# Kernel optimization log

Hardware: AMD Instinct MI355X
Metric: run time of the kernel (lower is better)

The kernel has to match this reference:

```python
import jax, jax.numpy as jnp
import numpy as np

# Model hyperparameters (from init_kwargs)
CHANNEL_COUNT = 32   # C: features per element
MIXTURE_COUNT = 4    # K: number of class distributions
MIXTURE_SIZE = 4     # S: gaussian components per class
EM_ITERS = 3         # fixed EM refinement iterations
LOG2PI = 1.8378770664093453
COV_REG = 1e-4       # covariance diagonal regularizer
EPS = 1e-6


def setup_inputs() -> dict:
    key = jax.random.key(0)
    kf, kl = jax.random.split(key)
    features = jax.random.normal(kf, (4, CHANNEL_COUNT, 65536), dtype=jnp.float32)
    initial_labels = jax.random.randint(kl, (4, 65536), 0, MIXTURE_COUNT, dtype=jnp.int32)
    return {"features": features, "initial_labels": initial_labels}


def reference(features, initial_labels):
    # features: [B, C, N] float; initial_labels: [B, N] int in [0, K)
    B, C, N = features.shape
    K, S = MIXTURE_COUNT, MIXTURE_SIZE
    dt = features.dtype

    # class membership mask [B, K, N]
    mask = jax.nn.one_hot(initial_labels, K, dtype=dt).transpose(0, 2, 1)
    # deterministic initial within-class component assignment: element n -> component n % S
    comp_onehot = jax.nn.one_hot(jnp.arange(N) % S, S, dtype=dt).T  # [S, N]
    r = mask[:, :, None, :] * comp_onehot[None, None]               # [B, K, S, N]

    eye = COV_REG * jnp.eye(C, dtype=dt)
    logp = None
    for _ in range(EM_ITERS):
        # ---- M-step: per-component weight, mean, covariance (sufficient stats) ----
        w = r.sum(-1)                                                # [B, K, S]
        mu = jnp.einsum('bksn,bcn->bksc', r, features) / (w[..., None] + EPS)
        sxx = jnp.einsum('bksn,bcn,bdn->bkscd', r, features, features) / (w[..., None, None] + EPS)
        cov = sxx - jnp.einsum('bksc,bksd->bkscd', mu, mu) + eye     # [B, K, S, C, C]
        prec = jnp.linalg.inv(cov)
        _, logdet = jnp.linalg.slogdet(cov)                          # [B, K, S]
        pi = (w + EPS) / (w.sum(-1, keepdims=True) + S * EPS)        # mixing weights

        # ---- E-step: full-covariance gaussian log-density per element ----
        t = jnp.einsum('bkscd,bdn->bkscn', prec, features)           # [B, K, S, C, N]
        quad = (jnp.einsum('bcn,bkscn->bksn', features, t)
                - 2.0 * jnp.einsum('bksc,bkscn->bksn', mu, t)
                + jnp.einsum('bksc,bkscd,bksd->bks', mu, prec, mu)[..., None])
        logp = jnp.log(pi)[..., None] - 0.5 * (C * LOG2PI + logdet[..., None] + quad)  # [B,K,S,N]
        # responsibilities within each class, restricted to that class's labeled elements
        r = jax.nn.softmax(logp, axis=2) * mask[:, :, None, :]

    # per-class mixture log-likelihood for EVERY element, then posterior over classes
    class_ll = jax.nn.logsumexp(logp, axis=2)        # [B, K, N]
    output_logits = jax.nn.softmax(class_ll, axis=1)  # class assignment probabilities
    return output_logits
```

## Files before the change

### kernel.cpp

```cpp
#include <hip/hip_runtime.h>
#include <hip/hip_fp16.h>
#include <math.h>

#define BB 4
#define CC 32
#define KK 4
#define SS 4
#define NN 65536

constexpr int NCOMP = 64;
constexpr int SSTRIDE = 1088;
constexpr int PSTRIDE = 1128;
constexpr int NB = 128;
constexpr float EPS_ = 1e-6f;
constexpr float COVREG_ = 1e-4f;
constexpr float LOG2PI_C = 1.8378770664093453f;

__device__ constexpr int XOFF_[32] = {
    0,   4,   8,   12,  16,  24,  32,  40,  48,  60,  72,
    84,  96,  112, 128, 144, 160, 180, 200, 220, 240, 264,
    288, 312, 336, 364, 392, 420, 448, 480, 512, 544};

typedef _Float16 half8 __attribute__((ext_vector_type(8)));
typedef _Float16 half4 __attribute__((ext_vector_type(4)));
typedef float floatx4 __attribute__((ext_vector_type(4)));

template <bool ITER0, int CHUNKS>
__global__ __launch_bounds__(256, 2) void gmm_accum_mfma(
    const float* __restrict__ feat, const int* __restrict__ labels,
    const float* __restrict__ resp, float* __restrict__ partials) {
  __shared__ __align__(16) _Float16 fC[32 * 48];
  __shared__ __align__(16) _Float16 respH[4][32];
  __shared__ __align__(16) _Float16 maskH[4][32];

  const int t = threadIdx.x;
  const int b = blockIdx.y;
  const int blk0 = blockIdx.x * (CHUNKS * 32);
  const int k = t >> 6;
  const int l = t & 63;
  const int row16 = l & 15;
  const int kg = l >> 4;

  floatx4 acc[4][7];
#pragma unroll
  for (int s = 0; s < 4; ++s)
#pragma unroll
    for (int j = 0; j < 7; ++j) acc[s][j] = (floatx4){0.f, 0.f, 0.f, 0.f};

  const int cstage = t >> 3;
  const int n4 = (t & 7) * 4;

  float4 pf;
  float4 presp = make_float4(0, 0, 0, 0);
  int plab = 0;
  pf = *(const float4*)(feat + ((size_t)b * CC + cstage) * NN + blk0 + n4);
  if (t < 32) {
    plab = labels[b * NN + blk0 + t];
    if (!ITER0) presp = *(const float4*)(resp + ((size_t)b * NN + blk0 + t) * 4);
  }

  const half8 hz = {0, 0, 0, 0, 0, 0, 0, 0};

  for (int chunk = 0; chunk < CHUNKS; ++chunk) {
    {
      half4 hv;
      hv[0] = (_Float16)pf.x;
      hv[1] = (_Float16)pf.y;
      hv[2] = (_Float16)pf.z;
      hv[3] = (_Float16)pf.w;
      *(half4*)&fC[cstage * 48 + n4] = hv;
    }
    if (t < 32) {
      if (ITER0) {
        const int cmp = (blk0 + chunk * 32 + t) & 3;
        respH[0][t] = (cmp == 0) ? (_Float16)1 : (_Float16)0;
        respH[1][t] = (cmp == 1) ? (_Float16)1 : (_Float16)0;
        respH[2][t] = (cmp == 2) ? (_Float16)1 : (_Float16)0;
        respH[3][t] = (cmp == 3) ? (_Float16)1 : (_Float16)0;
      } else {
        respH[0][t] = (_Float16)presp.x;
        respH[1][t] = (_Float16)presp.y;
        respH[2][t] = (_Float16)presp.z;
        respH[3][t] = (_Float16)presp.w;
      }
      maskH[0][t] = (plab == 0) ? (_Float16)1 : (_Float16)0;
      maskH[1][t] = (plab == 1) ? (_Float16)1 : (_Float16)0;
      maskH[2][t] = (plab == 2) ? (_Float16)1 : (_Float16)0;
      maskH[3][t] = (plab == 3) ? (_Float16)1 : (_Float16)0;
    }
    __syncthreads();

    if (chunk < CHUNKS - 1) {
      const int n0n = blk0 + (chunk + 1) * 32;
      pf = *(const float4*)(feat + ((size_t)b * CC + cstage) * NN + n0n + n4);
      if (t < 32) {
        plab = labels[b * NN + n0n + t];
        if (!ITER0)
          presp = *(const float4*)(resp + ((size_t)b * NN + n0n + t) * 4);
      }
    }

    const half8 ff0 = *(const half8*)&fC[row16 * 48 + kg * 8];
    const half8 ff1 = *(const half8*)&fC[(row16 + 16) * 48 + kg * 8];

    const half8 mh = *(const half8*)&maskH[k][kg * 8];
    const half8 H0 = ff0 * mh;
    const half8 H1 = ff1 * mh;
    const half8 agB = (row16 == 0) ? mh : hz;

#pragma unroll
    for (int s = 0; s < 4; ++s) {
      const half8 rh = *(const half8*)&respH[s][kg * 8];
      const half8 G0 = ff0 * rh;
      const half8 G1 = ff1 * rh;
      const half8 agA = (row16 == 0) ? rh : hz;
      acc[s][0] =
          __builtin_amdgcn_mfma_f32_16x16x32_f16(G0, H0, acc[s][0], 0, 0, 0);
      acc[s][1] =
          __builtin_amdgcn_mfma_f32_16x16x32_f16(G0, H1, acc[s][1], 0, 0, 0);
      acc[s][2] =
          __builtin_amdgcn_mfma_f32_16x16x32_f16(G1, H0, acc[s][2], 0, 0, 0);
      acc[s][3] =
          __builtin_amdgcn_mfma_f32_16x16x32_f16(G1, H1, acc[s][3], 0, 0, 0);
      acc[s][4] =
          __builtin_amdgcn_mfma_f32_16x16x32_f16(G0, agB, acc[s][4], 0, 0, 0);
      acc[s][5] =
          __builtin_amdgcn_mfma_f32_16x16x32_f16(G1, agB, acc[s][5], 0, 0, 0);
      acc[s][6] =
          __builtin_amdgcn_mfma_f32_16x16x32_f16(agA, agB, acc[s][6], 0, 0, 0);
    }
    __syncthreads();
  }

#pragma unroll
  for (int s = 0; s < 4; ++s) {
    float* sg = partials + ((size_t)(b * gridDim.x + blockIdx.x) * 16 +
                            (k * 4 + s)) *
                               SSTRIDE;
    const int dr = kg * 4;
#pragma unroll
    for (int r = 0; r < 4; ++r) {
      sg[(dr + r) * 32 + row16] = acc[s][0][r];
      sg[(dr + r) * 32 + 16 + row16] = acc[s][1][r];
      sg[(16 + dr + r) * 32 + row16] = acc[s][2][r];
      sg[(16 + dr + r) * 32 + 16 + row16] = acc[s][3][r];
    }
    if (row16 == 0) {
#pragma unroll
      for (int r = 0; r < 4; ++r) {
        sg[1024 + dr + r] = acc[s][4][r];
        sg[1024 + 16 + dr + r] = acc[s][5][r];
      }
    }
    if (l == 0) sg[1056] = acc[s][6][0];
  }
}

template <int TILES>
__global__ __launch_bounds__(256, 2) void gmm_fused(
    const float* __restrict__ feat, const int* __restrict__ labels,
    const float* __restrict__ params, float* __restrict__ partials) {
  __shared__ __align__(16) _Float16 fTd[2 * 64 * 56];
  __shared__ __align__(16) _Float16 fCd[2 * 32 * 72];
  __shared__ int4 xlds4[2048];
  __shared__ float zlds[16 * 32];
  __shared__ float c0lds[16];
  __shared__ int lab_lds[2][64];
  __shared__ __align__(16) _Float16 respHd[2][4][64];
  __shared__ __align__(16) _Float16 maskHd[2][4][64];

  const int t = threadIdx.x;
  const int b = blockIdx.y;
  const int blk0 = blockIdx.x * (TILES * 64);
  const int w = t >> 6;
  const int l = t & 63;
  const int row16 = l & 15;
  const int kg = l >> 4;

  for (int idx = t; idx < 2048; idx += 256) {
    const int c = idx >> 7, chunk = idx & 127;
    xlds4[idx] = *(const int4*)((const char*)(params +
                                              (size_t)(b * 16 + c) * PSTRIDE +
                                              612) +
                                chunk * 16);
  }
  for (int idx = t; idx < 16 * 32; idx += 256) {
    zlds[idx] =
        -params[(size_t)(b * 16 + (idx >> 5)) * PSTRIDE + 576 + (idx & 31)];
  }
  if (t < 16) c0lds[t] = params[(size_t)(b * 16 + t) * PSTRIDE + 608];

  const _Float16* xl = (const _Float16*)xlds4;
  const int cload = t >> 4;
  const int i4 = (t & 15) * 4;
  const half8 hz = {0, 0, 0, 0, 0, 0, 0, 0};

  floatx4 acc[4][7];
#pragma unroll
  for (int s = 0; s < 4; ++s)
#pragma unroll
    for (int j = 0; j < 7; ++j) acc[s][j] = (floatx4){0.f, 0.f, 0.f, 0.f};

  float4 pv0 = *(const float4*)(feat + ((size_t)b * CC + cload) * NN + blk0 + i4);
  float4 pv1 =
      *(const float4*)(feat + ((size_t)b * CC + cload + 16) * NN + blk0 + i4);
  int plab = (t < 64) ? labels[b * NN + blk0 + t] : 0;

  for (int tile = 0; tile < TILES; ++tile) {
    const int base = blk0 + tile * 64;
    const int bs = tile & 1;
    _Float16* fT = &fTd[bs * (64 * 56)];
    _Float16* fC = &fCd[bs * (32 * 72)];

    {
      const _Float16 h0x = (_Float16)pv0.x, h0y = (_Float16)pv0.y;
      const _Float16 h0z = (_Float16)pv0.z, h0w = (_Float16)pv0.w;
      const _Float16 h1x = (_Float16)pv1.x, h1y = (_Float16)pv1.y;
      const _Float16 h1z = (_Float16)pv1.z, h1w = (_Float16)pv1.w;
      fT[(i4 + 0) * 56 + cload] = h0x;
      fT[(i4 + 1) * 56 + cload] = h0y;
      fT[(i4 + 2) * 56 + cload] = h0z;
      fT[(i4 + 3) * 56 + cload] = h0w;
      fT[(i4 + 0) * 56 + cload + 16] = h1x;
      fT[(i4 + 1) * 56 + cload + 16] = h1y;
      fT[(i4 + 2) * 56 + cload + 16] = h1z;
      fT[(i4 + 3) * 56 + cload + 16] = h1w;
      half4 a, c2;
      a[0] = h0x; a[1] = h0y; a[2] = h0z; a[3] = h0w;
      c2[0] = h1x; c2[1] = h1y; c2[2] = h1z; c2[3] = h1w;
      *(half4*)&fC[cload * 72 + i4] = a;
      *(half4*)&fC[(cload + 16) * 72 + i4] = c2;
      if (t < 64) lab_lds[bs][t] = plab;
    }
    __syncthreads();

    if (tile < TILES - 1) {
      const int nb2 = base + 64;
      pv0 = *(const float4*)(feat + ((size_t)b * CC + cload) * NN + nb2 + i4);
      pv1 = *(const float4*)(feat + ((size_t)b * CC + cload + 16) * NN + nb2 +
                             i4);
      if (t < 64) plab = labels[b * NN + nb2 + t];
    }

    const half8 bfr = *(const half8*)&fT[(w * 16 + row16) * 56 + kg * 8];
    const int lab = lab_lds[bs][w * 16 + row16];

    float lp0 = 0.f, lp1 = 0.f, lp2 = 0.f, lp3 = 0.f;
#pragma unroll
    for (int c = 0; c < 16; ++c) {
      const half8 a0 = *(const half8*)&xl[c * 1024 + (0 * 64 + l) * 8];
      const half8 a1 = *(const half8*)&xl[c * 1024 + (1 * 64 + l) * 8];
      const floatx4 cin0 = *(const floatx4*)&zlds[c * 32 + kg * 4];
      const floatx4 cin1 = *(const floatx4*)&zlds[c * 32 + 16 + kg * 4];
      floatx4 y0 =
          __builtin_amdgcn_mfma_f32_16x16x32_f16(a0, bfr, cin0, 0, 0, 0);
      floatx4 y1 =
          __builtin_amdgcn_mfma_f32_16x16x32_f16(a1, bfr, cin1, 0, 0, 0);
      float q = 0.f;
      q = fmaf(y0[0], y0[0], q);
      q = fmaf(y0[1], y0[1], q);
      q = fmaf(y0[2], y0[2], q);
      q = fmaf(y0[3], y0[3], q);
      q = fmaf(y1[0], y1[0], q);
      q = fmaf(y1[1], y1[1], q);
      q = fmaf(y1[2], y1[2], q);
      q = fmaf(y1[3], y1[3], q);
      q += __shfl_xor(q, 16);
      q += __shfl_xor(q, 32);
      const float lp = c0lds[c] - 0.5f * q;
      const bool own = (c >> 2) == lab;
      const int s = c & 3;
      lp0 = (own && s == 0) ? lp : lp0;
      lp1 = (own && s == 1) ? lp : lp1;
      lp2 = (own && s == 2) ? lp : lp2;
      lp3 = (own && s == 3) ? lp : lp3;
    }

    {
      const float m = fmaxf(fmaxf(lp0, lp1), fmaxf(lp2, lp3));
      const float e0 = expf(lp0 - m), e1 = expf(lp1 - m);
      const float e2 = expf(lp2 - m), e3 = expf(lp3 - m);
      const float inv = 1.f / (e0 + e1 + e2 + e3);
      if (l < 16) {
        const int e = w * 16 + l;
        respHd[bs][0][e] = (_Float16)(e0 * inv);
        respHd[bs][1][e] = (_Float16)(e1 * inv);
        respHd[bs][2][e] = (_Float16)(e2 * inv);
        respHd[bs][3][e] = (_Float16)(e3 * inv);
      }
      if (t < 64) {
        const int lb2 = lab_lds[bs][t];
        maskHd[bs][0][t] = (lb2 == 0) ? (_Float16)1 : (_Float16)0;
        maskHd[bs][1][t] = (lb2 == 1) ? (_Float16)1 : (_Float16)0;
        maskHd[bs][2][t] = (lb2 == 2) ? (_Float16)1 : (_Float16)0;
        maskHd[bs][3][t] = (lb2 == 3) ? (_Float16)1 : (_Float16)0;
      }
    }
    __syncthreads();

#pragma unroll
    for (int h = 0; h < 2; ++h) {
      const int eb = h * 32;
      const half8 ff0 = *(const half8*)&fC[row16 * 72 + eb + kg * 8];
      const half8 ff1 = *(const half8*)&fC[(row16 + 16) * 72 + eb + kg * 8];

      const half8 mh = *(const half8*)&maskHd[bs][w][eb + kg * 8];
      const half8 H0 = ff0 * mh;
      const half8 H1 = ff1 * mh;
      const half8 agB = (row16 == 0) ? mh : hz;

#pragma unroll
      for (int s = 0; s < 4; ++s) {
        const half8 rh = *(const half8*)&respHd[bs][s][eb + kg * 8];
        const half8 G0 = ff0 * rh;
        const half8 G1 = ff1 * rh;
        const half8 agA = (row16 == 0) ? rh : hz;
        acc[s][0] =
            __builtin_amdgcn_mfma_f32_16x16x32_f16(G0, H0, acc[s][0], 0, 0, 0);
        acc[s][1] =
            __builtin_amdgcn_mfma_f32_16x16x32_f16(G0, H1, acc[s][1], 0, 0, 0);
        acc[s][2] =
            __builtin_amdgcn_mfma_f32_16x16x32_f16(G1, H0, acc[s][2], 0, 0, 0);
        acc[s][3] =
            __builtin_amdgcn_mfma_f32_16x16x32_f16(G1, H1, acc[s][3], 0, 0, 0);
        acc[s][4] =
            __builtin_amdgcn_mfma_f32_16x16x32_f16(G0, agB, acc[s][4], 0, 0, 0);
        acc[s][5] =
            __builtin_amdgcn_mfma_f32_16x16x32_f16(G1, agB, acc[s][5], 0, 0, 0);
        acc[s][6] = __builtin_amdgcn_mfma_f32_16x16x32_f16(agA, agB, acc[s][6],
                                                           0, 0, 0);
      }
    }
  }

#pragma unroll
  for (int s = 0; s < 4; ++s) {
    float* sg = partials + ((size_t)(b * gridDim.x + blockIdx.x) * 16 +
                            (w * 4 + s)) *
                               SSTRIDE;
    const int dr = kg * 4;
#pragma unroll
    for (int r = 0; r < 4; ++r) {
      sg[(dr + r) * 32 + row16] = acc[s][0][r];
      sg[(dr + r) * 32 + 16 + row16] = acc[s][1][r];
      sg[(16 + dr + r) * 32 + row16] = acc[s][2][r];
      sg[(16 + dr + r) * 32 + 16 + row16] = acc[s][3][r];
    }
    if (row16 == 0) {
#pragma unroll
      for (int r = 0; r < 4; ++r) {
        sg[1024 + dr + r] = acc[s][4][r];
        sg[1024 + 16 + dr + r] = acc[s][5][r];
      }
    }
    if (l == 0) sg[1056] = acc[s][6][0];
  }
}

__global__ __launch_bounds__(256) void gmm_reduce(const float* __restrict__ part,
                                                  float* __restrict__ stats,
                                                  int nb) {
  const int idx = blockIdx.x * 256 + threadIdx.x;
  if (idx >= NCOMP * 1057) return;
  const int comp = idx / 1057;
  const int cell = idx - comp * 1057;
  const int b = comp >> 4, cl = comp & 15;
  const float* src = part + ((size_t)(b * nb) * 16 + cl) * SSTRIDE + cell;
  const size_t stride = (size_t)16 * SSTRIDE;
  float s0 = 0.f, s1 = 0.f;
#pragma unroll 8
  for (int blk = 0; blk < nb; blk += 2) {
    s0 += src[(size_t)blk * stride];
    s1 += src[(size_t)(blk + 1) * stride];
  }
  stats[(size_t)comp * SSTRIDE + cell] = s0 + s1;
}

__global__ __launch_bounds__(64) void gmm_params(const float* __restrict__ stats,
                                                 float* __restrict__ params) {
  __shared__ float Xl[32 * 33];
  __shared__ float mul[32];

  const int t = threadIdx.x;
  const int i = t & 31;
  const int comp = blockIdx.x;
  const float* sg = stats + (size_t)comp * SSTRIDE;

  const float w = sg[1056];
  const float invw = 1.f / (w + EPS_);
  const float mu_i = sg[1024 + i] * invw;

  float a[32];
#pragma unroll
  for (int j4 = 0; j4 < 8; ++j4) {
    const float4 v = *(const float4*)(sg + i * 32 + 4 * j4);
    a[4 * j4 + 0] = v.x;
    a[4 * j4 + 1] = v.y;
    a[4 * j4 + 2] = v.z;
    a[4 * j4 + 3] = v.w;
  }
#pragma unroll
  for (int j = 0; j < 32; ++j) {
    const float muj = sg[1024 + j] * invw;
    float v = fmaf(a[j], invw, -mu_i * muj);
    v = (j == i) ? v + COVREG_ : v;
    a[j] = v;
  }

  float ldet = 0.f;
  float rd[32];
#pragma unroll
  for (int j = 0; j < 32; ++j) {
    const float diag = __shfl(a[j], j);
    ldet += logf(diag);
    const float rinv = rsqrtf(diag);
    rd[j] = rinv;
    const float lij = a[j] * rinv;
    a[j] = (i >= j) ? lij : a[j];
#pragma unroll
    for (int m = j + 1; m < 32; ++m) {
      const float Lmj = __shfl(lij, m);
      a[m] = (i >= m) ? fmaf(-lij, Lmj, a[m]) : a[m];
    }
  }

  float x[32];
#pragma unroll
  for (int m = 0; m < 32; ++m) {
    float s = (m == i) ? 1.f : 0.f;
#pragma unroll
    for (int r = 0; r < m; ++r) {
      const float Lmr = __shfl(a[r], m);
      s = fmaf(-Lmr, x[r], s);
    }
    x[m] = s * rd[m];
  }

  if (t < 32) {
#pragma unroll
    for (int m = 0; m < 32; ++m) Xl[m * 33 + i] = x[m];
    mul[i] = mu_i;
  }
  __syncthreads();

  float* pg = params + (size_t)comp * PSTRIDE;
  for (int r = 0; r < 32; ++r) {
    const int L4 = 4 * ((r >> 2) + 1);
    if (t < L4) pg[XOFF_[r] + t] = (t <= r) ? Xl[r * 33 + t] : 0.f;
  }
  {
    __half* xh = (__half*)(pg + 612);
#pragma unroll
    for (int th = 0; th < 2; ++th) {
      const int row = th * 16 + (t & 15);
      const int k0 = (t >> 4) * 8;
#pragma unroll
      for (int j = 0; j < 8; ++j) {
        const int k = k0 + j;
        const float v = (k <= row) ? Xl[row * 33 + k] : 0.f;
        xh[(th * 64 + t) * 8 + j] = __float2half(v);
      }
    }
  }
  if (t < 32) {
    float z = 0.f;
    for (int j = 0; j <= t; ++j) z += Xl[t * 33 + j] * mul[j];
    pg[576 + t] = z;
  }
  if (t == 0) {
    const int sib = comp & ~3;
    float wsum = 0.f;
    for (int s2 = 0; s2 < 4; ++s2)
      wsum += stats[(size_t)(sib + s2) * SSTRIDE + 1056];
    const float pi = (w + EPS_) / (wsum + SS * EPS_);
    pg[608] = logf(pi) - 0.5f * (CC * LOG2PI_C + ldet);
  }
}

template <int TILES>
__global__ __launch_bounds__(256, 2) void gmm_estep_final4(
    const float* __restrict__ feat, const float* __restrict__ params,
    float* __restrict__ out) {
  __shared__ __align__(16) _Float16 fTd[2 * 64 * 56];
  __shared__ int4 xlds4[2048];
  __shared__ float zlds[16 * 32];
  __shared__ float c0lds[16];

  const int t = threadIdx.x;
  const int b = blockIdx.y;
  const int blk0 = blockIdx.x * (TILES * 64);
  const int w = t >> 6;
  const int l = t & 63;
  const int row16 = l & 15;
  const int kg = l >> 4;

  for (int idx = t; idx < 2048; idx += 256) {
    const int c = idx >> 7, chunk = idx & 127;
    xlds4[idx] = *(const int4*)((const char*)(params +
                                              (size_t)(b * 16 + c) * PSTRIDE +
                                              612) +
                                chunk * 16);
  }
  for (int idx = t; idx < 16 * 32; idx += 256) {
    zlds[idx] =
        -params[(size_t)(b * 16 + (idx >> 5)) * PSTRIDE + 576 + (idx & 31)];
  }
  if (t < 16) c0lds[t] = params[(size_t)(b * 16 + t) * PSTRIDE + 608];

  const _Float16* xl = (const _Float16*)xlds4;
  const int cload = t >> 4;
  const int i4 = (t & 15) * 4;

  float4 pv0 = *(const float4*)(feat + ((size_t)b * CC + cload) * NN + blk0 + i4);
  float4 pv1 =
      *(const float4*)(feat + ((size_t)b * CC + cload + 16) * NN + blk0 + i4);

  for (int tile = 0; tile < TILES; ++tile) {
    const int base = blk0 + tile * 64;
    const int bs = tile & 1;
    _Float16* fT = &fTd[bs * (64 * 56)];
    {
      fT[(i4 + 0) * 56 + cload] = (_Float16)pv0.x;
      fT[(i4 + 1) * 56 + cload] = (_Float16)pv0.y;
      fT[(i4 + 2) * 56 + cload] = (_Float16)pv0.z;
      fT[(i4 + 3) * 56 + cload] = (_Float16)pv0.w;
      fT[(i4 + 0) * 56 + cload + 16] = (_Float16)pv1.x;
      fT[(i4 + 1) * 56 + cload + 16] = (_Float16)pv1.y;
      fT[(i4 + 2) * 56 + cload + 16] = (_Float16)pv1.z;
      fT[(i4 + 3) * 56 + cload + 16] = (_Float16)pv1.w;
    }
    __syncthreads();

    if (tile < TILES - 1) {
      const int nb2 = base + 64;
      pv0 = *(const float4*)(feat + ((size_t)b * CC + cload) * NN + nb2 + i4);
      pv1 = *(const float4*)(feat + ((size_t)b * CC + cload + 16) * NN + nb2 +
                             i4);
    }

    const half8 bfr = *(const half8*)&fT[(w * 16 + row16) * 56 + kg * 8];

    float lp[16];
#pragma unroll
    for (int c = 0; c < 16; ++c) {
      const half8 a0 = *(const half8*)&xl[c * 1024 + (0 * 64 + l) * 8];
      const half8 a1 = *(const half8*)&xl[c * 1024 + (1 * 64 + l) * 8];
      const floatx4 cin0 = *(const floatx4*)&zlds[c * 32 + kg * 4];
      const floatx4 cin1 = *(const floatx4*)&zlds[c * 32 + 16 + kg * 4];
      floatx4 y0 =
          __builtin_amdgcn_mfma_f32_16x16x32_f16(a0, bfr, cin0, 0, 0, 0);
      floatx4 y1 =
          __builtin_amdgcn_mfma_f32_16x16x32_f16(a1, bfr, cin1, 0, 0, 0);
      float q = 0.f;
      q = fmaf(y0[0], y0[0], q);
      q = fmaf(y0[1], y0[1], q);
      q = fmaf(y0[2], y0[2], q);
      q = fmaf(y0[3], y0[3], q);
      q = fmaf(y1[0], y1[0], q);
      q = fmaf(y1[1], y1[1], q);
      q = fmaf(y1[2], y1[2], q);
      q = fmaf(y1[3], y1[3], q);
      q += __shfl_xor(q, 16);
      q += __shfl_xor(q, 32);
      lp[c] = c0lds[c] - 0.5f * q;
    }

    float cll[4];
#pragma unroll
    for (int k = 0; k < 4; ++k) {
      const float m = fmaxf(fmaxf(lp[4 * k + 0], lp[4 * k + 1]),
                            fmaxf(lp[4 * k + 2], lp[4 * k + 3]));
      const float s = expf(lp[4 * k + 0] - m) + expf(lp[4 * k + 1] - m) +
                      expf(lp[4 * k + 2] - m) + expf(lp[4 * k + 3] - m);
      cll[k] = m + logf(s);
    }
    const float m = fmaxf(fmaxf(cll[0], cll[1]), fmaxf(cll[2], cll[3]));
    const float e0 = expf(cll[0] - m), e1 = expf(cll[1] - m);
    const float e2 = expf(cll[2] - m), e3 = expf(cll[3] - m);
    const float inv = 1.f / (e0 + e1 + e2 + e3);
    if (l < 16) {
      const int n = base + w * 16 + l;
      out[((size_t)b * KK + 0) * NN + n] = e0 * inv;
      out[((size_t)b * KK + 1) * NN + n] = e1 * inv;
      out[((size_t)b * KK + 2) * NN + n] = e2 * inv;
      out[((size_t)b * KK + 3) * NN + n] = e3 * inv;
    }
  }
}

template <bool ITER0, bool ATOMIC, int TILES>
__global__ __launch_bounds__(256, 1) void gmm_accum(
    const float* __restrict__ feat, const int* __restrict__ labels,
    const float* __restrict__ resp, float* __restrict__ outbuf) {
  __shared__ float fT[64 * 36];
  __shared__ float resp_lds[64 * 4];
  __shared__ int lab_lds[64];

  const int t = threadIdx.x;
  const int b = blockIdx.y;
  const int blk0 = blockIdx.x * (TILES * 64);

  const int wv = t >> 6;
  const int l = t & 63;
  const int sc = (t >> 4) & 3;
  const int p = t & 15;
  const int a0 = (p >> 2) * 8;
  const int b0 = (p & 3) * 8;

  float acc[8][8];
#pragma unroll
  for (int x = 0; x < 8; ++x)
#pragma unroll
    for (int y = 0; y < 8; ++y) acc[x][y] = 0.f;
  float sx[8] = {0, 0, 0, 0, 0, 0, 0, 0};
  float wacc = 0.f;

  const int cload = t >> 4;
  const int i4 = (t & 15) * 4;

  float4 pf0, pf1;
  float4 presp = make_float4(0, 0, 0, 0);
  int plab = 0;
  {
    const int n0 = blk0;
    pf0 = *(const float4*)(feat + ((size_t)b * CC + cload) * NN + n0 + i4);
    pf1 = *(const float4*)(feat + ((size_t)b * CC + cload + 16) * NN + n0 + i4);
    if (t < 64) {
      plab = labels[b * NN + n0 + t];
      if (!ITER0)
        presp = *(const float4*)(resp + ((size_t)b * NN + n0 + t) * 4);
    }
  }

  for (int tile = 0; tile < TILES; ++tile) {
    fT[(i4 + 0) * 36 + cload] = pf0.x;
    fT[(i4 + 1) * 36 + cload] = pf0.y;
    fT[(i4 + 2) * 36 + cload] = pf0.z;
    fT[(i4 + 3) * 36 + cload] = pf0.w;
    fT[(i4 + 0) * 36 + cload + 16] = pf1.x;
    fT[(i4 + 1) * 36 + cload + 16] = pf1.y;
    fT[(i4 + 2) * 36 + cload + 16] = pf1.z;
    fT[(i4 + 3) * 36 + cload + 16] = pf1.w;
    if (t < 64) {
      lab_lds[t] = plab;
      if (ITER0) {
        const int cmp = (blk0 + tile * 64 + t) & 3;
        resp_lds[t * 4 + 0] = (cmp == 0) ? 1.f : 0.f;
        resp_lds[t * 4 + 1] = (cmp == 1) ? 1.f : 0.f;
        resp_lds[t * 4 + 2] = (cmp == 2) ? 1.f : 0.f;
        resp_lds[t * 4 + 3] = (cmp == 3) ? 1.f : 0.f;
      } else {
        resp_lds[t * 4 + 0] = presp.x;
        resp_lds[t * 4 + 1] = presp.y;
        resp_lds[t * 4 + 2] = presp.z;
        resp_lds[t * 4 + 3] = presp.w;
      }
    }
    __syncthreads();
    if (tile < TILES - 1) {
      const int n0 = blk0 + (tile + 1) * 64;
      pf0 = *(const float4*)(feat + ((size_t)b * CC + cload) * NN + n0 + i4);
      pf1 =
          *(const float4*)(feat + ((size_t)b * CC + cload + 16) * NN + n0 + i4);
      if (t < 64) {
        plab = labels[b * NN + n0 + t];
        if (!ITER0)
          presp = *(const float4*)(resp + ((size_t)b * NN + n0 + t) * 4);
      }
    }

    unsigned long long m = __ballot(lab_lds[l] == wv);
    while (m) {
      const int i = __builtin_ctzll(m);
      m &= m - 1;
      const float rs = resp_lds[i * 4 + sc];
      const float4 ra0 = *(const float4*)&fT[i * 36 + a0];
      const float4 ra1 = *(const float4*)&fT[i * 36 + a0 + 4];
      const float4 rb0 = *(const float4*)&fT[i * 36 + b0];
      const float4 rb1 = *(const float4*)&fT[i * 36 + b0 + 4];
      const float ra[8] = {ra0.x, ra0.y, ra0.z, ra0.w,
                           ra1.x, ra1.y, ra1.z, ra1.w};
      const float rb[8] = {rb0.x, rb0.y, rb0.z, rb0.w,
                           rb1.x, rb1.y, rb1.z, rb1.w};
#pragma unroll
      for (int x = 0; x < 8; ++x) {
        const float v = rs * ra[x];
#pragma unroll
        for (int y = 0; y < 8; ++y) acc[x][y] = fmaf(v, rb[y], acc[x][y]);
      }
#pragma unroll
      for (int y = 0; y < 8; ++y) sx[y] = fmaf(rs, rb[y], sx[y]);
      wacc += rs;
    }
    __syncthreads();
  }

  if (ATOMIC) {
    float* sg = outbuf + ((size_t)(b * KK + wv) * SS + sc) * SSTRIDE;
#pragma unroll
    for (int x = 0; x < 8; ++x)
#pragma unroll
      for (int y = 0; y < 8; ++y)
        atomicAdd(sg + (a0 + x) * 32 + b0 + y, acc[x][y]);
    if (p < 4) {
#pragma unroll
      for (int y = 0; y < 8; ++y) atomicAdd(sg + 1024 + b0 + y, sx[y]);
    }
    if (p == 0) atomicAdd(sg + 1056, wacc);
  } else {
    const int nb = NN / (TILES * 64);
    float* sg = outbuf + ((size_t)(b * nb + blockIdx.x) * 16 + (wv * 4 + sc)) *
                             SSTRIDE;
#pragma unroll
    for (int x = 0; x < 8; ++x)
#pragma unroll
      for (int y = 0; y < 8; ++y) sg[(a0 + x) * 32 + b0 + y] = acc[x][y];
    if (p < 4) {
#pragma unroll
      for (int y = 0; y < 8; ++y) sg[1024 + b0 + y] = sx[y];
    }
    if (p == 0) sg[1056] = wacc;
  }
}

template <int TILES>
__global__ __launch_bounds__(256, 2) void gmm_estep_own4(
    const float* __restrict__ feat, const int* __restrict__ labels,
    const float* __restrict__ params, float* __restrict__ resp) {
  __shared__ float fT[64 * 36];
  __shared__ int4 xlds4[2048];
  __shared__ float zlds[16 * 32];
  __shared__ float c0lds[16];
  __shared__ int lab_lds[64];

  const int t = threadIdx.x;
  const int b = blockIdx.y;
  const int blk0 = blockIdx.x * (TILES * 64);
  const int w = t >> 6;
  const int l = t & 63;
  const int row16 = l & 15;
  const int kg = l >> 4;

  for (int idx = t; idx < 2048; idx += 256) {
    const int c = idx >> 7, chunk = idx & 127;
    xlds4[idx] = *(const int4*)((const char*)(params +
                                              (size_t)(b * 16 + c) * PSTRIDE +
                                              612) +
                                chunk * 16);
  }
  for (int idx = t; idx < 16 * 32; idx += 256) {
    zlds[idx] =
        -params[(size_t)(b * 16 + (idx >> 5)) * PSTRIDE + 576 + (idx & 31)];
  }
  if (t < 16) c0lds[t] = params[(size_t)(b * 16 + t) * PSTRIDE + 608];

  const _Float16* xl = (const _Float16*)xlds4;
  const int cload = t >> 4;
  const int i4 = (t & 15) * 4;

  for (int tile = 0; tile < TILES; ++tile) {
    const int base = blk0 + tile * 64;
    {
      const float4 v0 =
          *(const float4*)(feat + ((size_t)b * CC + cload) * NN + base + i4);
      const float4 v1 = *(const float4*)(feat +
                                         ((size_t)b * CC + cload + 16) * NN +
                                         base + i4);
      fT[(i4 + 0) * 36 + cload] = v0.x;
      fT[(i4 + 1) * 36 + cload] = v0.y;
      fT[(i4 + 2) * 36 + cload] = v0.z;
      fT[(i4 + 3) * 36 + cload] = v0.w;
      fT[(i4 + 0) * 36 + cload + 16] = v1.x;
      fT[(i4 + 1) * 36 + cload + 16] = v1.y;
      fT[(i4 + 2) * 36 + cload + 16] = v1.z;
      fT[(i4 + 3) * 36 + cload + 16] = v1.w;
      if (t < 64) lab_lds[t] = labels[b * NN + base + t];
    }
    __syncthreads();

    const int eoff = (w * 16 + row16) * 36 + kg * 8;
    const float4 fv0 = *(const float4*)&fT[eoff];
    const float4 fv1 = *(const float4*)&fT[eoff + 4];
    half8 bfr;
    bfr[0] = (_Float16)fv0.x;
    bfr[1] = (_Float16)fv0.y;
    bfr[2] = (_Float16)fv0.z;
    bfr[3] = (_Float16)fv0.w;
    bfr[4] = (_Float16)fv1.x;
    bfr[5] = (_Float16)fv1.y;
    bfr[6] = (_Float16)fv1.z;
    bfr[7] = (_Float16)fv1.w;

    const int lab = lab_lds[w * 16 + row16];

    float lp0 = 0.f, lp1 = 0.f, lp2 = 0.f, lp3 = 0.f;
#pragma unroll
    for (int c = 0; c < 16; ++c) {
      const half8 a0 = *(const half8*)&xl[c * 1024 + (0 * 64 + l) * 8];
      const half8 a1 = *(const half8*)&xl[c * 1024 + (1 * 64 + l) * 8];
      const floatx4 cin0 = *(const floatx4*)&zlds[c * 32 + kg * 4];
      const floatx4 cin1 = *(const floatx4*)&zlds[c * 32 + 16 + kg * 4];
      floatx4 y0 =
          __builtin_amdgcn_mfma_f32_16x16x32_f16(a0, bfr, cin0, 0, 0, 0);
      floatx4 y1 =
          __builtin_amdgcn_mfma_f32_16x16x32_f16(a1, bfr, cin1, 0, 0, 0);
      float q = 0.f;
      q = fmaf(y0[0], y0[0], q);
      q = fmaf(y0[1], y0[1], q);
      q = fmaf(y0[2], y0[2], q);
      q = fmaf(y0[3], y0[3], q);
      q = fmaf(y1[0], y1[0], q);
      q = fmaf(y1[1], y1[1], q);
      q = fmaf(y1[2], y1[2], q);
      q = fmaf(y1[3], y1[3], q);
      q += __shfl_xor(q, 16);
      q += __shfl_xor(q, 32);
      const float lp = c0lds[c] - 0.5f * q;
      const bool own = (c >> 2) == lab;
      const int s = c & 3;
      lp0 = (own && s == 0) ? lp : lp0;
      lp1 = (own && s == 1) ? lp : lp1;
      lp2 = (own && s == 2) ? lp : lp2;
      lp3 = (own && s == 3) ? lp : lp3;
    }

    const float m = fmaxf(fmaxf(lp0, lp1), fmaxf(lp2, lp3));
    const float e0 = expf(lp0 - m), e1 = expf(lp1 - m);
    const float e2 = expf(lp2 - m), e3 = expf(lp3 - m);
    const float inv = 1.f / (e0 + e1 + e2 + e3);
    if (l < 16) {
      *(float4*)(resp + ((size_t)b * NN + base + w * 16 + l) * 4) =
          make_float4(e0 * inv, e1 * inv, e2 * inv, e3 * inv);
    }
    __syncthreads();
  }
}

extern "C" void kernel_launch(void* const* d_in, const int* in_sizes, int n_in,
                              void* d_out, int out_size, void* d_ws,
                              size_t ws_size, hipStream_t stream) {
  const float* feat = (const float*)d_in[0];
  const int* labels = (const int*)d_in[1];
  float* out = (float*)d_out;

  float* stats = (float*)d_ws;
  float* params = stats + (size_t)NCOMP * SSTRIDE;
  float* resp_ws = params + (size_t)NCOMP * PSTRIDE;
  float* partials = resp_ws + (size_t)BB * NN * 4;

  const size_t base_need_f =
      (size_t)NCOMP * SSTRIDE + (size_t)NCOMP * PSTRIDE + (size_t)BB * NN * 4;
  const size_t need128 =
      (base_need_f + (size_t)BB * NB * 16 * SSTRIDE) * sizeof(float);
  const bool have_resp = ws_size >= base_need_f * sizeof(float);
  float* resp = have_resp ? resp_ws : out;

  const int reduce_blocks = (NCOMP * 1057 + 255) / 256;

  if (ws_size >= need128) {
    gmm_accum_mfma<true, 16>
        <<<dim3(NB, BB), 256, 0, stream>>>(feat, labels, out, partials);
    gmm_reduce<<<reduce_blocks, 256, 0, stream>>>(partials, stats, NB);
    gmm_params<<<NCOMP, 64, 0, stream>>>(stats, params);
    for (int it = 1; it < 3; ++it) {
      gmm_fused<8>
          <<<dim3(NB, BB), 256, 0, stream>>>(feat, labels, params, partials);
      gmm_reduce<<<reduce_blocks, 256, 0, stream>>>(partials, stats, NB);
      gmm_params<<<NCOMP, 64, 0, stream>>>(stats, params);
    }
    gmm_estep_final4<8><<<dim3(NN / 512, BB), 256, 0, stream>>>(feat, params,
                                                                out);
  } else {
    for (int it = 0; it < 3; ++it) {
      hipMemsetAsync(stats, 0, (size_t)NCOMP * SSTRIDE * sizeof(float), stream);
      if (it == 0)
        gmm_accum<true, true, 16>
            <<<dim3(64, BB), 256, 0, stream>>>(feat, labels, resp, stats);
      else
        gmm_accum<false, true, 16>
            <<<dim3(64, BB), 256, 0, stream>>>(feat, labels, resp, stats);
      gmm_params<<<NCOMP, 64, 0, stream>>>(stats, params);
      if (it < 2)
        gmm_estep_own4<8><<<dim3(NN / 512, BB), 256, 0, stream>>>(feat, labels,
                                                                  params, resp);
      else
        gmm_estep_final4<8><<<dim3(NN / 512, BB), 256, 0, stream>>>(
            feat, params, out);
    }
  }
}
```

Measured before the change: 252.9 us.

## Fuse partial-sum reduction with per-component parameter computation into one kernel

Replaces the separate reduce and params kernels with a single kernel per component that sums block partials into shared memory, then does a Cholesky factorization, triangular inverse and log-determinant in-wavefront and writes the params. This removes one launch per EM iteration and the round-trip of stats through global memory. The trade-off is that the reduction now runs on only 64 blocks instead of roughly 265, which lowers memory-level parallelism for reading the partials.

```diff
diff --git a/kernel.cpp b/kernel.cpp
--- a/kernel.cpp
+++ b/kernel.cpp
@@ -357,6 +357,139 @@
   }
 }
 
+__global__ __launch_bounds__(256) void gmm_reduce_params(
+    const float* __restrict__ part, float* __restrict__ params, int nb) {
+  __shared__ float sl[1060];
+  __shared__ float wpart[4][32];
+  __shared__ float wsib[4];
+  __shared__ float Xl[32 * 33];
+  __shared__ float mul[32];
+
+  const int t = threadIdx.x;
+  const int comp = blockIdx.x;
+  const int b = comp >> 4, cl = comp & 15;
+  const size_t stride = (size_t)16 * SSTRIDE;
+  const float* src0 = part + ((size_t)(b * nb) * 16 + cl) * SSTRIDE;
+
+  for (int cell = t; cell < 1057; cell += 256) {
+    const float* src = src0 + cell;
+    float s0 = 0.f, s1 = 0.f;
+#pragma unroll 8
+    for (int blk = 0; blk < nb; blk += 2) {
+      s0 += src[(size_t)blk * stride];
+      s1 += src[(size_t)(blk + 1) * stride];
+    }
+    sl[cell] = s0 + s1;
+  }
+  if (t < 128) {
+    const int sib = (cl & ~3) + (t >> 5);
+    const int lane = t & 31;
+    const float* srcw =
+        part + ((size_t)(b * nb) * 16 + sib) * SSTRIDE + 1056;
+    float s = 0.f;
+    for (int q = lane; q < nb; q += 32) s += srcw[(size_t)q * stride];
+    wpart[t >> 5][lane] = s;
+  }
+  __syncthreads();
+  if (t < 4) {
+    float s = 0.f;
+#pragma unroll
+    for (int j = 0; j < 32; ++j) s += wpart[t][j];
+    wsib[t] = s;
+  }
+
+  float ldet = 0.f;
+  if (t < 64) {
+    const int i = t & 31;
+    const float w = sl[1056];
+    const float invw = 1.f / (w + EPS_);
+    const float mu_i = sl[1024 + i] * invw;
+
+    float a[32];
+#pragma unroll
+    for (int j4 = 0; j4 < 8; ++j4) {
+      const float4 v = *(const float4*)(sl + i * 32 + 4 * j4);
+      a[4 * j4 + 0] = v.x;
+      a[4 * j4 + 1] = v.y;
+      a[4 * j4 + 2] = v.z;
+      a[4 * j4 + 3] = v.w;
+    }
+#pragma unroll
+    for (int j = 0; j < 32; ++j) {
+      const float muj = sl[1024 + j] * invw;
+      float v = fmaf(a[j], invw, -mu_i * muj);
+      v = (j == i) ? v + COVREG_ : v;
+      a[j] = v;
+    }
+
+    float rd[32];
+#pragma unroll
+    for (int j = 0; j < 32; ++j) {
+      const float diag = __shfl(a[j], j);
+      ldet += logf(diag);
+      const float rinv = rsqrtf(diag);
+      rd[j] = rinv;
+      const float lij = a[j] * rinv;
+      a[j] = (i >= j) ? lij : a[j];
+#pragma unroll
+      for (int m = j + 1; m < 32; ++m) {
+        const float Lmj = __shfl(lij, m);
+        a[m] = (i >= m) ? fmaf(-lij, Lmj, a[m]) : a[m];
+      }
+    }
+
+    float x[32];
+#pragma unroll
+    for (int m = 0; m < 32; ++m) {
+      float s = (m == i) ? 1.f : 0.f;
+#pragma unroll
+      for (int r = 0; r < m; ++r) {
+        const float Lmr = __shfl(a[r], m);
+        s = fmaf(-Lmr, x[r], s);
+      }
+      x[m] = s * rd[m];
+    }
+
+    if (t < 32) {
+#pragma unroll
+      for (int m = 0; m < 32; ++m) Xl[m * 33 + i] = x[m];
+      mul[i] = mu_i;
+    }
+  }
+  __syncthreads();
+
+  float* pg = params + (size_t)comp * PSTRIDE;
+  for (int r = 0; r < 32; ++r) {
+    const int L4 = 4 * ((r >> 2) + 1);
+    if (t < L4) pg[XOFF_[r] + t] = (t <= r) ? Xl[r * 33 + t] : 0.f;
+  }
+  if (t < 64) {
+    __half* xh = (__half*)(pg + 612);
+#pragma unroll
+    for (int th = 0; th < 2; ++th) {
+      const int row = th * 16 + (t & 15);
+      const int k0 = (t >> 4) * 8;
+#pragma unroll
+      for (int j = 0; j < 8; ++j) {
+        const int k = k0 + j;
+        const float v = (k <= row) ? Xl[row * 33 + k] : 0.f;
+        xh[(th * 64 + t) * 8 + j] = __float2half(v);
+      }
+    }
+  }
+  if (t < 32) {
+    float z = 0.f;
+    for (int j = 0; j <= t; ++j) z += Xl[t * 33 + j] * mul[j];
+    pg[576 + t] = z;
+  }
+  if (t == 0) {
+    const float w = sl[1056];
+    const float wsum = wsib[0] + wsib[1] + wsib[2] + wsib[3];
+    const float pi = (w + EPS_) / (wsum + SS * EPS_);
+    pg[608] = logf(pi) - 0.5f * (CC * LOG2PI_C + ldet);
+  }
+}
+
 __global__ __launch_bounds__(256) void gmm_reduce(const float* __restrict__ part,
                                                   float* __restrict__ stats,
                                                   int nb) {
@@ -855,18 +988,14 @@
   const bool have_resp = ws_size >= base_need_f * sizeof(float);
   float* resp = have_resp ? resp_ws : out;
 
-  const int reduce_blocks = (NCOMP * 1057 + 255) / 256;
-
   if (ws_size >= need128) {
     gmm_accum_mfma<true, 16>
         <<<dim3(NB, BB), 256, 0, stream>>>(feat, labels, out, partials);
-    gmm_reduce<<<reduce_blocks, 256, 0, stream>>>(partials, stats, NB);
-    gmm_params<<<NCOMP, 64, 0, stream>>>(stats, params);
+    gmm_reduce_params<<<NCOMP, 256, 0, stream>>>(partials, params, NB);
     for (int it = 1; it < 3; ++it) {
       gmm_fused<8>
           <<<dim3(NB, BB), 256, 0, stream>>>(feat, labels, params, partials);
-      gmm_reduce<<<reduce_blocks, 256, 0, stream>>>(partials, stats, NB);
-      gmm_params<<<NCOMP, 64, 0, stream>>>(stats, params);
+      gmm_reduce_params<<<NCOMP, 256, 0, stream>>>(partials, params, NB);
     }
     gmm_estep_final4<8><<<dim3(NN / 512, BB), 256, 0, stream>>>(feat, params,
                                                                 out);
```

After: 343.9 us. 1.36x slower.
